# Performance work log

Hardware: AMD Instinct MI355X
Metric: run time of the kernel (lower is better)

## Reference

```python
import jax, jax.numpy as jnp
import numpy as np

N_EMBD = 384
N_HEAD = 6
HEAD_DIM = N_EMBD // N_HEAD


def setup_inputs() -> dict:
    key = jax.random.key(0)
    k1, k2, k3, k4, k5 = jax.random.split(key, 5)
    B, T, C = 256, 165, N_EMBD
    x = jax.random.normal(k1, (B, T, C), dtype=jnp.float32)
    # nn.Linear stores weight as [out, in]; we keep [in, out] for x @ W
    s = 1.0 / np.sqrt(C)
    w_qkv = jax.random.uniform(k2, (C, 3 * C), minval=-s, maxval=s, dtype=jnp.float32)
    b_qkv = jax.random.uniform(k3, (3 * C,), minval=-s, maxval=s, dtype=jnp.float32)
    w_proj = jax.random.uniform(k4, (C, C), minval=-s, maxval=s, dtype=jnp.float32)
    b_proj = jax.random.uniform(k5, (C,), minval=-s, maxval=s, dtype=jnp.float32)
    return {"x": x, "w_qkv": w_qkv, "b_qkv": b_qkv, "w_proj": w_proj, "b_proj": b_proj}


def _attn(x, w_qkv, b_qkv, w_proj, b_proj):
    B, T, C = x.shape
    qkv = x @ w_qkv + b_qkv                      # [B, T, 3C]
    q, k, v = jnp.split(qkv, 3, axis=-1)
    def heads(t):
        return t.reshape(B, T, N_HEAD, HEAD_DIM).transpose(0, 2, 1, 3)  # [B,H,T,D]
    q, k, v = heads(q), heads(k), heads(v)
    scale = 1.0 / np.sqrt(HEAD_DIM)
    scores = jnp.einsum("bhqd,bhkd->bhqk", q, k) * scale  # [B,H,T,T]
    # mask: all True except last row attends only to the last column
    row = jnp.arange(T)[:, None]
    col = jnp.arange(T)[None, :]
    allowed = (row != T - 1) | (col == T - 1)              # [T,T] bool
    scores = jnp.where(allowed, scores, -jnp.inf)
    attn = jax.nn.softmax(scores, axis=-1)
    y = jnp.einsum("bhqk,bhkd->bhqd", attn, v)             # [B,H,T,D]
    y = y.transpose(0, 2, 1, 3).reshape(B, T, C)
    return y @ w_proj + b_proj


def reference(x, w_qkv, b_qkv, w_proj, b_proj):
    return _attn(x, w_qkv, b_qkv, w_proj, b_proj)
```

## Files before the change

### kernel.cpp

```cpp
#include <hip/hip_runtime.h>


typedef __attribute__((ext_vector_type(8))) short s16x8;
typedef __attribute__((ext_vector_type(4))) float f32x4;

__device__ __forceinline__ ushort f2b(float f) {
  union { float f; unsigned u; } v; v.f = f;
  unsigned u = v.u;
  return (ushort)((u + 0x7FFFu + ((u >> 16) & 1u)) >> 16);
}

__device__ __forceinline__ void gload_lds16(const ushort* g, ushort* l) {
  __builtin_amdgcn_global_load_lds((const __attribute__((address_space(1))) void*)g,
                                   (__attribute__((address_space(3))) void*)l, 16, 0, 0);
}

__global__ __launch_bounds__(256) void prep(const float* __restrict__ x,
                                            const float* __restrict__ wq,
                                            const float* __restrict__ wp,
                                            ushort* __restrict__ xb,
                                            ushort* __restrict__ wqT,
                                            ushort* __restrict__ wpT)
{
  const int stride = gridDim.x * 256;
  const int i0 = blockIdx.x * 256 + threadIdx.x;
  for (int i = i0; i < 4055040; i += stride) {
    float4 v = ((const float4*)x)[i];
    ushort4 h = make_ushort4(f2b(v.x), f2b(v.y), f2b(v.z), f2b(v.w));
    ((ushort4*)xb)[i] = h;
  }
  for (int i = i0; i < 110592; i += stride) {
    const int n = i / 96, k4 = (i % 96) * 4;
    ushort4 h = make_ushort4(f2b(wq[(size_t)(k4 + 0) * 1152 + n]),
                             f2b(wq[(size_t)(k4 + 1) * 1152 + n]),
                             f2b(wq[(size_t)(k4 + 2) * 1152 + n]),
                             f2b(wq[(size_t)(k4 + 3) * 1152 + n]));
    *(ushort4*)(wqT + (size_t)n * 384 + k4) = h;
  }
  for (int i = i0; i < 36864; i += stride) {
    const int n = i / 96, k4 = (i % 96) * 4;
    ushort4 h = make_ushort4(f2b(wp[(size_t)(k4 + 0) * 384 + n]),
                             f2b(wp[(size_t)(k4 + 1) * 384 + n]),
                             f2b(wp[(size_t)(k4 + 2) * 384 + n]),
                             f2b(wp[(size_t)(k4 + 3) * 384 + n]));
    *(ushort4*)(wpT + (size_t)n * 384 + k4) = h;
  }
}

template<int NOUT, bool OUT_F32>
__global__ __launch_bounds__(256) void gemm_bias(const ushort* __restrict__ A,
                                                 const ushort* __restrict__ Bt,
                                                 const float* __restrict__ bias,
                                                 void* __restrict__ Out)
{
  __shared__ __align__(16) ushort Asm[128][64];
  __shared__ __align__(16) ushort Bsm[128][64];
  const int tid  = threadIdx.x;
  const int lane = tid & 63;
  const int wave = tid >> 6;
  const int wr = wave >> 1, wc = wave & 1;
  const int n0 = blockIdx.x * 128;
  const int m0 = blockIdx.y * 128;

  const ushort* Ag = A  + (size_t)(m0 + (tid >> 3)) * 384 + ((tid & 7) << 3);
  const ushort* Bg = Bt + (size_t)(n0 + (tid >> 3)) * 384 + ((tid & 7) << 3);
  ushort* AsmT = (ushort*)Asm + tid * 8;
  ushort* BsmT = (ushort*)Bsm + tid * 8;

  f32x4 acc[4][4] = {};

  for (int k0 = 0; k0 < 384; k0 += 64) {
    #pragma unroll
    for (int i = 0; i < 4; ++i) {
      gload_lds16(Ag + k0 + i * 32 * 384, AsmT + i * 2048);
      gload_lds16(Bg + k0 + i * 32 * 384, BsmT + i * 2048);
    }
    __syncthreads();
    #pragma unroll
    for (int ks = 0; ks < 2; ++ks) {
      const int kk = (ks << 5) + ((lane >> 4) << 3);
      s16x8 a[4], b[4];
      #pragma unroll
      for (int mi = 0; mi < 4; ++mi)
        a[mi] = *(const s16x8*)(&Asm[(wr << 6) + (mi << 4) + (lane & 15)][kk]);
      #pragma unroll
      for (int ni = 0; ni < 4; ++ni)
        b[ni] = *(const s16x8*)(&Bsm[(wc << 6) + (ni << 4) + (lane & 15)][kk]);
      #pragma unroll
      for (int mi = 0; mi < 4; ++mi) {
        #pragma unroll
        for (int ni = 0; ni < 4; ++ni)
          acc[mi][ni] = __builtin_amdgcn_mfma_f32_16x16x32_bf16(a[mi], b[ni], acc[mi][ni], 0, 0, 0);
      }
    }
    __syncthreads();
  }
  #pragma unroll
  for (int mi = 0; mi < 4; ++mi) {
    #pragma unroll
    for (int ni = 0; ni < 4; ++ni) {
      const int col = n0 + (wc << 6) + (ni << 4) + (lane & 15);
      const float bv = bias[col];
      #pragma unroll
      for (int r = 0; r < 4; ++r) {
        const int row = m0 + (wr << 6) + (mi << 4) + ((lane >> 4) << 2) + r;
        const float v = acc[mi][ni][r] + bv;
        if (OUT_F32) ((float*)Out)[(size_t)row * NOUT + col] = v;
        else         ((ushort*)Out)[(size_t)row * NOUT + col] = f2b(v);
      }
    }
  }
}

__global__ __launch_bounds__(256) void attn_kernel(const ushort* __restrict__ QKV,
                                                   ushort* __restrict__ Y)
{
  __shared__ __align__(16) ushort Ksm[165][64];
  __shared__ __align__(16) ushort Vtsm[64][168];
  __shared__ __align__(16) ushort Psm[4][16][168];
  const int bh = blockIdx.x;
  const int b = bh / 6, h = bh % 6;
  const int tid = threadIdx.x, lane = tid & 63, wave = tid >> 6;
  const size_t base = (size_t)b * 165 * 1152 + (size_t)h * 64;

  for (int idx = tid; idx < 165 * 8; idx += 256) {
    const int t = idx >> 3, d8 = (idx & 7) << 3;
    *(uint4*)(&Ksm[t][d8]) = *(const uint4*)(QKV + base + (size_t)t * 1152 + 384 + d8);
  }
  for (int idx = tid; idx < 165 * 8; idx += 256) {
    const int t = idx >> 3, d8 = (idx & 7) << 3;
    uint4 v = *(const uint4*)(QKV + base + (size_t)t * 1152 + 768 + d8);
    const ushort* pv = (const ushort*)&v;
    #pragma unroll
    for (int j = 0; j < 8; ++j) Vtsm[d8 + j][t] = pv[j];
  }
  for (int idx = tid; idx < 64 * 3; idx += 256) Vtsm[idx / 3][165 + idx % 3] = 0;
  __syncthreads();

  const int colv = lane & 15;
  const int grp  = lane >> 4;
  for (int it = 0; it < 3; ++it) {
    const int qt = wave + (it << 2);
    const bool active = qt < 11;
    if (active) {
      const int tq = qt * 16 + colv;
      const int tqc = tq > 164 ? 164 : tq;
      const ushort* qrow = QKV + base + (size_t)tqc * 1152;
      const s16x8 qf0 = *(const s16x8*)(qrow + (grp << 3));
      const s16x8 qf1 = *(const s16x8*)(qrow + 32 + (grp << 3));
      f32x4 s[11];
      #pragma unroll
      for (int ct = 0; ct < 11; ++ct) {
        const int col = ct * 16 + colv;
        s16x8 kb0 = {}, kb1 = {};
        if (col < 165) {
          kb0 = *(const s16x8*)(&Ksm[col][grp << 3]);
          kb1 = *(const s16x8*)(&Ksm[col][32 + (grp << 3)]);
        }
        f32x4 a = {};
        a = __builtin_amdgcn_mfma_f32_16x16x32_bf16(qf0, kb0, a, 0, 0, 0);
        a = __builtin_amdgcn_mfma_f32_16x16x32_bf16(qf1, kb1, a, 0, 0, 0);
        s[ct] = a * 0.125f;
      }
      #pragma unroll
      for (int r = 0; r < 4; ++r) {
        float m = -1e30f;
        #pragma unroll
        for (int ct = 0; ct < 11; ++ct)
          if (ct * 16 + colv < 165) m = fmaxf(m, s[ct][r]);
        #pragma unroll
        for (int off = 1; off < 16; off <<= 1) m = fmaxf(m, __shfl_xor(m, off));
        float sum = 0.f;
        #pragma unroll
        for (int ct = 0; ct < 11; ++ct) {
          const float p = (ct * 16 + colv < 165) ? __expf(s[ct][r] - m) : 0.f;
          s[ct][r] = p;
          sum += p;
        }
        #pragma unroll
        for (int off = 1; off < 16; off <<= 1) sum += __shfl_xor(sum, off);
        const float inv = 1.f / sum;
        #pragma unroll
        for (int ct = 0; ct < 11; ++ct) s[ct][r] *= inv;
      }
      #pragma unroll
      for (int ct = 0; ct < 11; ++ct) {
        const int col = ct * 16 + colv;
        if (col < 168) {
          #pragma unroll
          for (int r = 0; r < 4; ++r)
            Psm[wave][(grp << 2) + r][col] = f2b(s[ct][r]);
        }
      }
    }
    __syncthreads();
    if (active) {
      f32x4 ya[4] = {};
      #pragma unroll
      for (int ksv = 0; ksv < 6; ++ksv) {
        const int kk = (ksv << 5) + (grp << 3);
        s16x8 pa = {};
        if (kk <= 160) pa = *(const s16x8*)(&Psm[wave][colv][kk]);
        #pragma unroll
        for (int nt = 0; nt < 4; ++nt) {
          s16x8 vb = {};
          if (kk <= 160) vb = *(const s16x8*)(&Vtsm[nt * 16 + colv][kk]);
          ya[nt] = __builtin_amdgcn_mfma_f32_16x16x32_bf16(pa, vb, ya[nt], 0, 0, 0);
        }
      }
      #pragma unroll
      for (int nt = 0; nt < 4; ++nt) {
        #pragma unroll
        for (int r = 0; r < 4; ++r) {
          const int trow = qt * 16 + (grp << 2) + r;
          if (trow < 165) {
            const int d = nt * 16 + colv;
            ushort val;
            if (trow == 164) val = QKV[base + (size_t)164 * 1152 + 768 + d];
            else             val = f2b(ya[nt][r]);
            Y[((size_t)b * 165 + trow) * 384 + h * 64 + d] = val;
          }
        }
      }
    }
    __syncthreads();
  }
}

extern "C" void kernel_launch(void* const* d_in, const int* in_sizes, int n_in,
                              void* d_out, int out_size, void* d_ws, size_t ws_size,
                              hipStream_t stream) {
  const float* x      = (const float*)d_in[0];
  const float* w_qkv  = (const float*)d_in[1];
  const float* b_qkv  = (const float*)d_in[2];
  const float* w_proj = (const float*)d_in[3];
  const float* b_proj = (const float*)d_in[4];
  float* out = (float*)d_out;

  char* ws = (char*)d_ws;
  ushort* xb  = (ushort*)ws;
  ushort* wqT = (ushort*)(ws + 32440320);
  ushort* wpT = (ushort*)(ws + 33325056);
  ushort* qkv = (ushort*)(ws + 33619968);
  ushort* y   = xb;

  prep<<<1024, 256, 0, stream>>>(x, w_qkv, w_proj, xb, wqT, wpT);
  gemm_bias<1152, false><<<dim3(9, 330), 256, 0, stream>>>(xb, wqT, b_qkv, qkv);
  attn_kernel<<<1536, 256, 0, stream>>>(qkv, y);
  gemm_bias<384, true><<<dim3(3, 330), 256, 0, stream>>>(y, wpT, b_proj, out);
}
```

Baseline: 288.5 us.

## Double-buffer GEMM LDS loads and remap blocks for XCD locality

```diff
diff --git a/kernel.cpp b/kernel.cpp
--- a/kernel.cpp
+++ b/kernel.cpp
@@ -47,45 +47,64 @@
   }
 }
 
-template<int NOUT, bool OUT_F32>
+template<int NB, int NOUT, bool OUT_F32>
 __global__ __launch_bounds__(256) void gemm_bias(const ushort* __restrict__ A,
                                                  const ushort* __restrict__ Bt,
                                                  const float* __restrict__ bias,
                                                  void* __restrict__ Out)
 {
-  __shared__ __align__(16) ushort Asm[128][64];
-  __shared__ __align__(16) ushort Bsm[128][64];
+  __shared__ __align__(16) ushort Asm[2][128][64];
+  __shared__ __align__(16) ushort Bsm[2][128][64];
   const int tid  = threadIdx.x;
   const int lane = tid & 63;
   const int wave = tid >> 6;
   const int wr = wave >> 1, wc = wave & 1;
-  const int n0 = blockIdx.x * 128;
-  const int m0 = blockIdx.y * 128;
+
+  const int nwg = gridDim.x;
+  const int qch = nwg >> 3, rch = nwg & 7;
+  const int xcd = blockIdx.x & 7, idx = blockIdx.x >> 3;
+  const int nl = (xcd < rch) ? xcd * (qch + 1) + idx
+                             : rch * (qch + 1) + (xcd - rch) * qch + idx;
+  const int n0 = (nl % NB) * 128;
+  const int m0 = (nl / NB) * 128;
 
   const ushort* Ag = A  + (size_t)(m0 + (tid >> 3)) * 384 + ((tid & 7) << 3);
   const ushort* Bg = Bt + (size_t)(n0 + (tid >> 3)) * 384 + ((tid & 7) << 3);
-  ushort* AsmT = (ushort*)Asm + tid * 8;
-  ushort* BsmT = (ushort*)Bsm + tid * 8;
 
   f32x4 acc[4][4] = {};
 
-  for (int k0 = 0; k0 < 384; k0 += 64) {
-    #pragma unroll
-    for (int i = 0; i < 4; ++i) {
-      gload_lds16(Ag + k0 + i * 32 * 384, AsmT + i * 2048);
-      gload_lds16(Bg + k0 + i * 32 * 384, BsmT + i * 2048);
-    }
-    __syncthreads();
+#define STAGE(buf, k0)                                              \
+  {                                                                 \
+    ushort* at_ = (ushort*)Asm[buf] + tid * 8;                      \
+    ushort* bt_ = (ushort*)Bsm[buf] + tid * 8;                      \
+    _Pragma("unroll")                                               \
+    for (int i = 0; i < 4; ++i) {                                   \
+      gload_lds16(Ag + (k0) + i * 32 * 384, at_ + i * 2048);        \
+      gload_lds16(Bg + (k0) + i * 32 * 384, bt_ + i * 2048);        \
+    }                                                               \
+  }
+
+  STAGE(0, 0);
+  #pragma unroll
+  for (int t = 0; t < 6; ++t) {
+    const int cur = t & 1;
+    if (t < 5) {
+      STAGE(cur ^ 1, (t + 1) * 64);
+      asm volatile("s_waitcnt vmcnt(8)" ::: "memory");
+    } else {
+      asm volatile("s_waitcnt vmcnt(0)" ::: "memory");
+    }
+    __builtin_amdgcn_s_barrier();
     #pragma unroll
     for (int ks = 0; ks < 2; ++ks) {
       const int kk = (ks << 5) + ((lane >> 4) << 3);
       s16x8 a[4], b[4];
       #pragma unroll
       for (int mi = 0; mi < 4; ++mi)
-        a[mi] = *(const s16x8*)(&Asm[(wr << 6) + (mi << 4) + (lane & 15)][kk]);
+        a[mi] = *(const s16x8*)(&Asm[cur][(wr << 6) + (mi << 4) + (lane & 15)][kk]);
       #pragma unroll
       for (int ni = 0; ni < 4; ++ni)
-        b[ni] = *(const s16x8*)(&Bsm[(wc << 6) + (ni << 4) + (lane & 15)][kk]);
+        b[ni] = *(const s16x8*)(&Bsm[cur][(wc << 6) + (ni << 4) + (lane & 15)][kk]);
       #pragma unroll
       for (int mi = 0; mi < 4; ++mi) {
         #pragma unroll
@@ -93,8 +112,10 @@
           acc[mi][ni] = __builtin_amdgcn_mfma_f32_16x16x32_bf16(a[mi], b[ni], acc[mi][ni], 0, 0, 0);
       }
     }
-    __syncthreads();
-  }
+    __builtin_amdgcn_s_barrier();
+  }
+#undef STAGE
+
   #pragma unroll
   for (int mi = 0; mi < 4; ++mi) {
     #pragma unroll
@@ -245,7 +266,7 @@
   ushort* y   = xb;
 
   prep<<<1024, 256, 0, stream>>>(x, w_qkv, w_proj, xb, wqT, wpT);
-  gemm_bias<1152, false><<<dim3(9, 330), 256, 0, stream>>>(xb, wqT, b_qkv, qkv);
+  gemm_bias<9, 1152, false><<<2970, 256, 0, stream>>>(xb, wqT, b_qkv, qkv);
   attn_kernel<<<1536, 256, 0, stream>>>(qkv, y);
-  gemm_bias<384, true><<<dim3(3, 330), 256, 0, stream>>>(y, wpT, b_proj, out);
-}
+  gemm_bias<3, 384, true><<<990, 256, 0, stream>>>(y, wpT, b_proj, out);
+}
```

Measured after the change: 261.2 us. 1.1x faster.
